# Kernel optimization log

Measured on AMD Instinct MI355X. Metric: run time of the kernel, lower is better.

The kernel has to match this reference:

```python
import jax, jax.numpy as jnp
import numpy as np

# Model dims (ViT-Base @ 384)
L, H, D, HD, M, P, IMG, B, NC, CH = 12, 12, 768, 64, 3072, 16, 384, 32, 1000, 3
NPATCH = (IMG // P) ** 2  # 576
SCALE = 1.0 / np.sqrt(HD)


def setup_inputs() -> dict:
    key = jax.random.key(0)
    ks = iter(jax.random.split(key, 16))
    def n(shape, s=0.02):
        return (jax.random.normal(next(ks), shape, jnp.float32) * s).astype(jnp.float32)
    return dict(
        x=jax.random.normal(next(ks), (B, CH, IMG, IMG), jnp.float32),
        conv_w=n((D, CH, P, P)), conv_b=jnp.zeros((D,), jnp.float32),
        cls_token=jnp.zeros((1, 1, D), jnp.float32),
        pos_emb=n((1, NPATCH + 1, D), 1.0),
        ln1_g=jnp.ones((L, D), jnp.float32), ln1_b=jnp.zeros((L, D), jnp.float32),
        wqkv=n((L, H, D, 3 * HD)), bqkv=jnp.zeros((L, H, 3 * HD), jnp.float32),
        wmsa=n((L, D, D)), bmsa=jnp.zeros((L, D), jnp.float32),
        ln2_g=jnp.ones((L, D), jnp.float32), ln2_b=jnp.zeros((L, D), jnp.float32),
        lnm_g=jnp.ones((L, D), jnp.float32), lnm_b=jnp.zeros((L, D), jnp.float32),
        w1=n((L, D, M)), b1=jnp.zeros((L, M), jnp.float32),
        w2=n((L, M, D)), b2=jnp.zeros((L, D), jnp.float32),
        lnf_g=jnp.ones((D,), jnp.float32), lnf_b=jnp.zeros((D,), jnp.float32),
        whead=n((D, NC)), bhead=jnp.zeros((NC,), jnp.float32),
    )


def _ln(x, g, b, eps=1e-5):
    mu = jnp.mean(x, axis=-1, keepdims=True)
    var = jnp.mean(jnp.square(x - mu), axis=-1, keepdims=True)
    return (x - mu) * jax.lax.rsqrt(var + eps) * g + b


def _encoder_block(x, p):
    (ln1_g, ln1_b, wqkv, bqkv, wmsa, bmsa,
     ln2_g, ln2_b, lnm_g, lnm_b, w1, b1, w2, b2) = p
    b = x.shape[0]
    h = _ln(x, ln1_g, ln1_b)
    # batched per-head QKV (math identical to looping over H small Linears)
    qkv = jnp.einsum('bsd,hde->bhse', h, wqkv) + bqkv[:, None, :]  # [B,H,S,3*HD]
    q, k, v = jnp.split(qkv, 3, axis=-1)
    attn = jax.nn.softmax(jnp.einsum('bhqe,bhke->bhqk', q, k) * SCALE, axis=-1)
    o = jnp.einsum('bhqk,bhke->bhqe', attn, v)          # [B,H,S,HD]
    o = o.transpose(0, 2, 1, 3).reshape(b, -1, D)        # concat heads along feature
    msa = jnp.einsum('bsd,de->bse', o, wmsa) + bmsa
    x1 = h + msa                                          # residual around MSA (post-LN1)
    h2 = _ln(x1, ln2_g, ln2_b)
    h2 = _ln(h2, lnm_g, lnm_b)                            # MLPBlock's own LayerNorm (double LN, faithful)
    mlp = jnp.einsum('bsm,md->bsd', jax.nn.gelu(jnp.einsum('bsd,dm->bsm', h2, w1) + b1, approximate=False), w2) + b2
    return x1 + mlp, None


def reference(x, conv_w, conv_b, cls_token, pos_emb,
              ln1_g, ln1_b, wqkv, bqkv, wmsa, bmsa,
              ln2_g, ln2_b, lnm_g, lnm_b, w1, b1, w2, b2,
              lnf_g, lnf_b, whead, bhead):
    b = x.shape[0]
    # patchify conv (image divisible by patch, so F.pad is a no-op)
    t = jax.lax.conv_general_dilated(x, conv_w, (P, P), 'VALID',
                                     dimension_numbers=('NCHW', 'OIHW', 'NCHW'))
    t = t + conv_b[None, :, None, None]
    # faithful to torch .view(b, -1, embed_dim) on NCHW layout (channel-major flatten)
    t = t.reshape(b, -1, D)
    n = t.shape[1]
    t = jnp.concatenate([jnp.broadcast_to(cls_token, (b, 1, D)), t], axis=1)
    t = t + pos_emb[:, :n + 1]
    stacked = (ln1_g, ln1_b, wqkv, bqkv, wmsa, bmsa,
               ln2_g, ln2_b, lnm_g, lnm_b, w1, b1, w2, b2)
    t, _ = jax.lax.scan(_encoder_block, t, stacked)
    y = _ln(t[:, 0], lnf_g, lnf_b)
    y = jax.nn.softmax(jnp.einsum('bd,dc->bc', y, whead) + bhead, axis=-1)
    return y
```

## Files before the change

kernel.cpp:

```cpp
#include <hip/hip_runtime.h>

using f16   = _Float16;
using f16x8 = __attribute__((ext_vector_type(8))) _Float16;
using f32x4 = __attribute__((ext_vector_type(4))) float;

#define MPAD  18560
#define MREAL 18464
#define MCONV 18432
#define SEQ   577
#define SPAD  640
#define NHEAD 12
#define NBATCH 32
#define SCALE_ 0.125f

__device__ __forceinline__ void load_lds16(const void* g, void* l) {
  __builtin_amdgcn_global_load_lds(
      (const __attribute__((address_space(1))) void*)g,
      (__attribute__((address_space(3))) void*)l, 16, 0, 0);
}

template<int K, int EPI>
__global__ __launch_bounds__(256) void gemm_k(
    const f16* __restrict__ A, const f16* __restrict__ Bt,
    const float* __restrict__ bias, const float* __restrict__ res,
    float* __restrict__ o32, f16* __restrict__ o16a, f16* __restrict__ o16b,
    f16* __restrict__ o16c, const float* __restrict__ pos, int N, int Mreal)
{
  __shared__ __align__(16) f16 As[128*32];
  __shared__ __align__(16) f16 Bs[128*32];
  const int tid = threadIdx.x;
  const int lane = tid & 63, wv = tid >> 6;

  const int gx = gridDim.x, gy = gridDim.y;
  const int nwg = gx * gy;
  const int flat = blockIdx.y * gx + blockIdx.x;
  const int xcd = flat & 7;
  const int qq = nwg >> 3, rr = nwg & 7;
  const int p_ = ((xcd < rr) ? xcd * (qq + 1) : rr * (qq + 1) + (xcd - rr) * qq)
                 + (flat >> 3);
  const int bandsz = gy * 6;
  const int band = p_ / bandsz, within = p_ - band * bandsz;
  const int byi = within / 6;
  const int bxi = band * 6 + (within - byi * 6);
  const int bm = byi << 7, bn = bxi << 7;

  const int wm = (wv >> 1) << 6, wn = (wv & 1) << 6;
  const int r16 = lane & 15, g4 = lane >> 4;
  const f32x4 Z4 = {0.f, 0.f, 0.f, 0.f};

  f32x4 acc[4][4];
#pragma unroll
  for (int m = 0; m < 4; ++m)
#pragma unroll
    for (int n = 0; n < 4; ++n) acc[m][n] = Z4;

  const int soff = wv * 1024 + lane * 8;
  for (int k0 = 0; k0 < K; k0 += 32) {
#pragma unroll
    for (int j = 0; j < 2; ++j) {
      int off = soff + j * 512;
      int row = off >> 5;
      int cs  = (off >> 3) & 3;
      int gc  = cs ^ (row & 3);
      load_lds16(A  + (size_t)(bm + row) * K + k0 + gc * 8, As + (wv*2 + j) * 512);
      load_lds16(Bt + (size_t)(bn + row) * K + k0 + gc * 8, Bs + (wv*2 + j) * 512);
    }
    __syncthreads();
    f16x8 af[4], bf[4];
#pragma unroll
    for (int m = 0; m < 4; ++m) {
      int row = wm + m * 16 + r16;
      af[m] = *(const f16x8*)(As + row * 32 + ((g4 ^ (row & 3)) << 3));
    }
#pragma unroll
    for (int n = 0; n < 4; ++n) {
      int row = wn + n * 16 + r16;
      bf[n] = *(const f16x8*)(Bs + row * 32 + ((g4 ^ (row & 3)) << 3));
    }
#pragma unroll
    for (int m = 0; m < 4; ++m)
#pragma unroll
      for (int n = 0; n < 4; ++n)
        acc[m][n] = __builtin_amdgcn_mfma_f32_16x16x32_f16(af[m], bf[n], acc[m][n], 0, 0, 0);
    __syncthreads();
  }

#pragma unroll
  for (int m = 0; m < 4; ++m) {
#pragma unroll
    for (int n = 0; n < 4; ++n) {
#pragma unroll
      for (int r = 0; r < 4; ++r) {
        int grow = bm + wm + m * 16 + g4 * 4 + r;
        int gcol = bn + wn + n * 16 + r16;
        float v = acc[m][n][r];
        if constexpr (EPI == 0) {
          if (grow < Mreal) {
            int b = grow / 576, p = grow - b * 576;
            int i = gcol * 576 + p;
            int sp = i / 768, dd = i - sp * 768;
            o32[((size_t)(b * SEQ + sp + 1)) * 768 + dd] =
                v + bias[gcol] + pos[(size_t)(sp + 1) * 768 + dd];
          }
        } else if constexpr (EPI == 1) {
          if (grow < Mreal) {
            int b = grow / SEQ, s = grow - b * SEQ;
            int hq = gcol / 192, rem = gcol - hq * 192;
            int sel = rem >> 6, e = rem & 63;
            float val = v + bias[gcol];
            int bh = b * NHEAD + hq;
            if (sel == 0)      o16a[((size_t)bh * SPAD + s) * 64 + e] = (f16)val;
            else if (sel == 1) o16b[((size_t)bh * SPAD + s) * 64 + e] = (f16)val;
            else               o16c[((size_t)bh * 64 + e) * SPAD + s] = (f16)val;
          }
        } else if constexpr (EPI == 2) {
          size_t idx = (size_t)grow * N + gcol;
          o32[idx] = v + bias[gcol] + res[idx];
        } else {
          float val = v + bias[gcol];
          float gl = 0.5f * val * (1.0f + erff(val * 0.70710678f));
          o16a[(size_t)grow * N + gcol] = (f16)gl;
        }
      }
    }
  }
}

__device__ __forceinline__ void block_red2(float& a, float& b, float* sm, int tid) {
  __syncthreads();
#pragma unroll
  for (int d = 32; d; d >>= 1) { a += __shfl_down(a, d); b += __shfl_down(b, d); }
  if ((tid & 63) == 0) { int w = tid >> 6; sm[w] = a; sm[w + 4] = b; }
  __syncthreads();
  a = sm[0] + sm[1] + sm[2] + sm[3];
  b = sm[4] + sm[5] + sm[6] + sm[7];
}

__global__ __launch_bounds__(256) void ln_fwd(const float* __restrict__ X,
    const float* __restrict__ g, const float* __restrict__ bb,
    float* __restrict__ ho, f16* __restrict__ hh)
{
  int row = blockIdx.x, tid = threadIdx.x;
  const float* x = X + (size_t)row * 768;
  float v0 = x[tid], v1 = x[tid + 256], v2 = x[tid + 512];
  float s = v0 + v1 + v2, s2 = v0*v0 + v1*v1 + v2*v2;
  __shared__ float sm[8];
  block_red2(s, s2, sm, tid);
  float mu = s * (1.f/768.f);
  float var = s2 * (1.f/768.f) - mu * mu;
  float rs = rsqrtf(var + 1e-5f);
  size_t base = (size_t)row * 768;
  float y0 = (v0 - mu) * rs * g[tid      ] + bb[tid      ];
  float y1 = (v1 - mu) * rs * g[tid + 256] + bb[tid + 256];
  float y2 = (v2 - mu) * rs * g[tid + 512] + bb[tid + 512];
  ho[base + tid] = y0; ho[base + tid + 256] = y1; ho[base + tid + 512] = y2;
  hh[base + tid] = (f16)y0; hh[base + tid + 256] = (f16)y1; hh[base + tid + 512] = (f16)y2;
}

__global__ __launch_bounds__(256) void ln2_fwd(const float* __restrict__ X,
    const float* __restrict__ g2, const float* __restrict__ bb2,
    const float* __restrict__ gm, const float* __restrict__ bbm,
    f16* __restrict__ hh)
{
  int row = blockIdx.x, tid = threadIdx.x;
  const float* x = X + (size_t)row * 768;
  float v0 = x[tid], v1 = x[tid + 256], v2 = x[tid + 512];
  float s = v0 + v1 + v2, s2 = v0*v0 + v1*v1 + v2*v2;
  __shared__ float sm[8];
  block_red2(s, s2, sm, tid);
  float mu = s * (1.f/768.f), var = s2 * (1.f/768.f) - mu * mu;
  float rs = rsqrtf(var + 1e-5f);
  float y0 = (v0 - mu) * rs * g2[tid      ] + bb2[tid      ];
  float y1 = (v1 - mu) * rs * g2[tid + 256] + bb2[tid + 256];
  float y2 = (v2 - mu) * rs * g2[tid + 512] + bb2[tid + 512];
  s = y0 + y1 + y2; s2 = y0*y0 + y1*y1 + y2*y2;
  block_red2(s, s2, sm, tid);
  mu = s * (1.f/768.f); var = s2 * (1.f/768.f) - mu * mu;
  rs = rsqrtf(var + 1e-5f);
  size_t base = (size_t)row * 768;
  hh[base + tid      ] = (f16)((y0 - mu) * rs * gm[tid      ] + bbm[tid      ]);
  hh[base + tid + 256] = (f16)((y1 - mu) * rs * gm[tid + 256] + bbm[tid + 256]);
  hh[base + tid + 512] = (f16)((y2 - mu) * rs * gm[tid + 512] + bbm[tid + 512]);
}

__global__ __launch_bounds__(256) void attn_k(const f16* __restrict__ qbuf,
    const f16* __restrict__ kbuf, const f16* __restrict__ vtbuf,
    f16* __restrict__ obuf)
{
  const int bh = blockIdx.y;
  const int b = bh / NHEAD, hd = bh - b * NHEAD;
  const int s0 = blockIdx.x << 6;
  const int tid = threadIdx.x, lane = tid & 63, wv = tid >> 6;
  const int r16 = lane & 15, g4 = lane >> 4;
  const f16* Q  = qbuf  + (size_t)bh * SPAD * 64;
  const f16* Kg = kbuf  + (size_t)bh * SPAD * 64;
  const f16* Vg = vtbuf + (size_t)bh * 64 * SPAD;
  __shared__ __align__(16) f16 Kt[64 * 64];
  __shared__ __align__(16) f16 Vt[64 * 64];
  __shared__ __align__(16) f16 Pw[4][16][72];
  const f32x4 Z4 = {0.f, 0.f, 0.f, 0.f};

  f16x8 qf[2];
  {
    const f16* qr = Q + (size_t)(s0 + wv * 16 + r16) * 64;
    qf[0] = *(const f16x8*)(qr + g4 * 8);
    qf[1] = *(const f16x8*)(qr + 32 + g4 * 8);
  }
  float m_run[4] = {-1e30f, -1e30f, -1e30f, -1e30f};
  float l_run[4] = {0.f, 0.f, 0.f, 0.f};
  f32x4 o_acc[4];
#pragma unroll
  for (int n = 0; n < 4; ++n) o_acc[n] = Z4;

  for (int kt = 0; kt < SPAD; kt += 64) {
#pragma unroll
    for (int j = 0; j < 2; ++j) {
      int off = (wv * 2 + j) * 1024 + lane * 16;
      int row = off >> 7;
      int cs  = (off >> 4) & 7;
      int gc  = cs ^ (row & 7);
      load_lds16(Kg + (size_t)(kt + row) * 64 + gc * 8, (void*)((char*)Kt + (wv*2 + j) * 1024));
      load_lds16(Vg + (size_t)row * SPAD + kt + gc * 8, (void*)((char*)Vt + (wv*2 + j) * 1024));
    }
    __syncthreads();

    f32x4 sa[4];
#pragma unroll
    for (int n = 0; n < 4; ++n) sa[n] = Z4;
#pragma unroll
    for (int n = 0; n < 4; ++n) {
      int krow = n * 16 + r16;
#pragma unroll
      for (int kc = 0; kc < 2; ++kc) {
        f16x8 kf = *(const f16x8*)(Kt + krow * 64 + (((kc * 4 + g4) ^ (krow & 7)) << 3));
        sa[n] = __builtin_amdgcn_mfma_f32_16x16x32_f16(qf[kc], kf, sa[n], 0, 0, 0);
      }
    }
#pragma unroll
    for (int r = 0; r < 4; ++r) {
      float mx = -1e30f;
#pragma unroll
      for (int n = 0; n < 4; ++n) {
        int key = kt + n * 16 + r16;
        float sv = (key < SEQ) ? sa[n][r] * SCALE_ : -1e30f;
        sa[n][r] = sv;
        mx = fmaxf(mx, sv);
      }
#pragma unroll
      for (int d = 1; d < 16; d <<= 1) mx = fmaxf(mx, __shfl_xor(mx, d));
      float mnew = fmaxf(m_run[r], mx);
      float alpha = __expf(m_run[r] - mnew);
      m_run[r] = mnew;
      float ssum = 0.f;
#pragma unroll
      for (int n = 0; n < 4; ++n) {
        float p = __expf(sa[n][r] - mnew);
        ssum += p;
        Pw[wv][g4 * 4 + r][n * 16 + r16] = (f16)p;
      }
#pragma unroll
      for (int d = 1; d < 16; d <<= 1) ssum += __shfl_xor(ssum, d);
      l_run[r] = l_run[r] * alpha + ssum;
#pragma unroll
      for (int n = 0; n < 4; ++n) o_acc[n][r] *= alpha;
    }
    f16x8 pf[2];
    pf[0] = *(const f16x8*)(&Pw[wv][r16][g4 * 8]);
    pf[1] = *(const f16x8*)(&Pw[wv][r16][32 + g4 * 8]);
#pragma unroll
    for (int n = 0; n < 4; ++n) {
      int erow = n * 16 + r16;
#pragma unroll
      for (int kc = 0; kc < 2; ++kc) {
        f16x8 vf = *(const f16x8*)(Vt + erow * 64 + (((kc * 4 + g4) ^ (erow & 7)) << 3));
        o_acc[n] = __builtin_amdgcn_mfma_f32_16x16x32_f16(pf[kc], vf, o_acc[n], 0, 0, 0);
      }
    }
    __syncthreads();
  }
  float inv[4];
#pragma unroll
  for (int r = 0; r < 4; ++r) inv[r] = 1.f / l_run[r];
#pragma unroll
  for (int n = 0; n < 4; ++n)
#pragma unroll
    for (int r = 0; r < 4; ++r) {
      int s = s0 + wv * 16 + g4 * 4 + r;
      if (s < SEQ)
        obuf[((size_t)(b * SEQ + s)) * 768 + hd * 64 + n * 16 + r16] =
            (f16)(o_acc[n][r] * inv[r]);
    }
}

__global__ __launch_bounds__(256) void cvt_transpose(const float* __restrict__ in,
    f16* __restrict__ out, int K, int N, size_t ls_in, size_t ls_out)
{
  in  += (size_t)blockIdx.z * ls_in;
  out += (size_t)blockIdx.z * ls_out;
  __shared__ float t[32][33];
  int n0 = blockIdx.x << 5, k0 = blockIdx.y << 5;
  int tx = threadIdx.x & 31, ty = threadIdx.x >> 5;
#pragma unroll
  for (int i = 0; i < 4; ++i) t[ty + 8*i][tx] = in[(size_t)(k0 + ty + 8*i) * N + n0 + tx];
  __syncthreads();
#pragma unroll
  for (int i = 0; i < 4; ++i) out[(size_t)(n0 + ty + 8*i) * K + k0 + tx] = (f16)t[tx][ty + 8*i];
}

__global__ __launch_bounds__(256) void cvt_qkvw(const float* __restrict__ in,
    f16* __restrict__ out, size_t ls_in, size_t ls_out)
{
  in  += (size_t)blockIdx.z * ls_in;
  out += (size_t)blockIdx.z * ls_out;
  __shared__ float t[32][33];
  int n0 = blockIdx.x << 5, k0 = blockIdx.y << 5;
  int tx = threadIdx.x & 31, ty = threadIdx.x >> 5;
  int hq = n0 / 192, r0 = n0 - hq * 192;
#pragma unroll
  for (int i = 0; i < 4; ++i)
    t[ty + 8*i][tx] = in[(size_t)hq * 147456 + (size_t)(k0 + ty + 8*i) * 192 + r0 + tx];
  __syncthreads();
#pragma unroll
  for (int i = 0; i < 4; ++i) out[(size_t)(n0 + ty + 8*i) * 768 + k0 + tx] = (f16)t[tx][ty + 8*i];
}

__global__ __launch_bounds__(256) void cvt_plain(const float* __restrict__ in,
    f16* __restrict__ out, int n)
{
  int i = blockIdx.x * 1024 + threadIdx.x;
#pragma unroll
  for (int j = 0; j < 4; ++j) { int idx = i + j * 256; if (idx < n) out[idx] = (f16)in[idx]; }
}

__global__ __launch_bounds__(256) void zero_vpad(f16* __restrict__ vtb) {
  int bh = blockIdx.x;
  for (int idx = threadIdx.x; idx < 64 * (SPAD - SEQ); idx += 256) {
    int e = idx / (SPAD - SEQ), s = SEQ + idx - e * (SPAD - SEQ);
    vtb[((size_t)bh * 64 + e) * SPAD + s] = (f16)0.f;
  }
}

__global__ __launch_bounds__(256) void im2col_k(const float* __restrict__ x, f16* __restrict__ out) {
  int row = blockIdx.x;
  int b = row / 576, p = row - b * 576;
  int py = p / 24, px = p - py * 24;
  int tid = threadIdx.x;
#pragma unroll
  for (int j = 0; j < 3; ++j) {
    int k = tid + j * 256;
    int c = k >> 8, rem = k & 255;
    int iy = rem >> 4, ix = rem & 15;
    out[(size_t)row * 768 + k] =
        (f16)x[(((size_t)(b * 3 + c)) * 384 + py * 16 + iy) * 384 + px * 16 + ix];
  }
}

__global__ __launch_bounds__(256) void cls_k(const float* __restrict__ ct,
    const float* __restrict__ pos, float* __restrict__ X)
{
  int b = blockIdx.x, tid = threadIdx.x;
#pragma unroll
  for (int j = 0; j < 3; ++j) {
    int d0 = tid + j * 256;
    X[((size_t)b * SEQ) * 768 + d0] = ct[d0] + pos[d0];
  }
}

__global__ __launch_bounds__(256) void head_k(const float* __restrict__ X,
    const float* __restrict__ g, const float* __restrict__ bb,
    const float* __restrict__ W, const float* __restrict__ bhd,
    float* __restrict__ out)
{
  int b = blockIdx.x, tid = threadIdx.x;
  const float* x = X + (size_t)(b * SEQ) * 768;
  float v0 = x[tid], v1 = x[tid + 256], v2 = x[tid + 512];
  float s = v0 + v1 + v2, s2 = v0*v0 + v1*v1 + v2*v2;
  __shared__ float sm[8];
  block_red2(s, s2, sm, tid);
  float mu = s * (1.f/768.f), var = s2 * (1.f/768.f) - mu * mu;
  float rs = rsqrtf(var + 1e-5f);
  __shared__ float y[768];
  y[tid      ] = (v0 - mu) * rs * g[tid      ] + bb[tid      ];
  y[tid + 256] = (v1 - mu) * rs * g[tid + 256] + bb[tid + 256];
  y[tid + 512] = (v2 - mu) * rs * g[tid + 512] + bb[tid + 512];
  __syncthreads();
  float lg[4];
#pragma unroll
  for (int j = 0; j < 4; ++j) {
    int c = tid + j * 256;
    float acc = (c < 1000) ? bhd[c] : -1e30f;
    if (c < 1000)
      for (int d = 0; d < 768; ++d) acc = fmaf(y[d], W[(size_t)d * 1000 + c], acc);
    lg[j] = acc;
  }
  float mx = fmaxf(fmaxf(lg[0], lg[1]), fmaxf(lg[2], lg[3]));
#pragma unroll
  for (int d = 32; d; d >>= 1) mx = fmaxf(mx, __shfl_down(mx, d));
  if ((tid & 63) == 0) sm[tid >> 6] = mx;
  __syncthreads();
  mx = fmaxf(fmaxf(sm[0], sm[1]), fmaxf(sm[2], sm[3]));
  float ex[4], se = 0.f;
#pragma unroll
  for (int j = 0; j < 4; ++j) {
    int c = tid + j * 256;
    ex[j] = (c < 1000) ? __expf(lg[j] - mx) : 0.f;
    se += ex[j];
  }
  __syncthreads();
#pragma unroll
  for (int d = 32; d; d >>= 1) se += __shfl_down(se, d);
  if ((tid & 63) == 0) sm[tid >> 6] = se;
  __syncthreads();
  se = sm[0] + sm[1] + sm[2] + sm[3];
  float inv = 1.f / se;
#pragma unroll
  for (int j = 0; j < 4; ++j) {
    int c = tid + j * 256;
    if (c < 1000) out[(size_t)b * 1000 + c] = ex[j] * inv;
  }
}

extern "C" void kernel_launch(void* const* d_in, const int* in_sizes, int n_in,
                              void* d_out, int out_size, void* d_ws, size_t ws_size,
                              hipStream_t stream)
{
  (void)in_sizes; (void)n_in; (void)out_size;
  const float* x      = (const float*)d_in[0];
  const float* conv_w = (const float*)d_in[1];
  const float* conv_b = (const float*)d_in[2];
  const float* cls_t  = (const float*)d_in[3];
  const float* pos    = (const float*)d_in[4];
  const float* ln1_g  = (const float*)d_in[5];
  const float* ln1_b  = (const float*)d_in[6];
  const float* wqkv   = (const float*)d_in[7];
  const float* bqkv   = (const float*)d_in[8];
  const float* wmsa   = (const float*)d_in[9];
  const float* bmsa   = (const float*)d_in[10];
  const float* ln2_g  = (const float*)d_in[11];
  const float* ln2_b  = (const float*)d_in[12];
  const float* lnm_g  = (const float*)d_in[13];
  const float* lnm_b  = (const float*)d_in[14];
  const float* w1     = (const float*)d_in[15];
  const float* b1     = (const float*)d_in[16];
  const float* w2     = (const float*)d_in[17];
  const float* b2     = (const float*)d_in[18];
  const float* lnf_g  = (const float*)d_in[19];
  const float* lnf_b  = (const float*)d_in[20];
  const float* whead  = (const float*)d_in[21];
  const float* bhead  = (const float*)d_in[22];
  float* out = (float*)d_out;

  const size_t szQ  = (size_t)2304 * 768;
  const size_t szM  = (size_t)768 * 768;
  const size_t szW1 = (size_t)3072 * 768;
  const size_t szW2 = (size_t)768 * 3072;
  const size_t fixed_bytes =
      (size_t)MPAD * 768 * 4 + (size_t)MPAD * 768 * 4 + (size_t)MPAD * 768 * 2 +
      (size_t)MPAD * 3072 * 2 + 3 * ((size_t)NBATCH * NHEAD * SPAD * 64 * 2) +
      (size_t)768 * 768 * 2  + 16 * 256 ;
  const bool hoist =
      ws_size >= fixed_bytes + 12 * (szQ + szM + szW1 + szW2) * 2 + 8 * 256;
  const int LW = hoist ? 12 : 1;

  char* wsp = (char*)d_ws;
  size_t off = 0;
  auto alloc = [&](size_t bytes) {
    char* p = wsp + off; off += (bytes + 255) & ~(size_t)255; return p;
  };
  float* X    = (float*)alloc((size_t)MPAD * 768 * 4);
  float* hbf  = (float*)alloc((size_t)MPAD * 768 * 4);
  f16*   hh   = (f16*)  alloc((size_t)MPAD * 768 * 2);
  f16*   abuf = (f16*)  alloc((size_t)MPAD * 3072 * 2);
  f16*   qb   = (f16*)  alloc((size_t)NBATCH * NHEAD * SPAD * 64 * 2);
  f16*   kb   = (f16*)  alloc((size_t)NBATCH * NHEAD * SPAD * 64 * 2);
  f16*   vtb  = (f16*)  alloc((size_t)NBATCH * NHEAD * SPAD * 64 * 2);
  f16*   WcT  = (f16*)  alloc((size_t)768 * 768 * 2);
  f16*   WqkvT= (f16*)  alloc(LW * szQ  * 2);
  f16*   WmsaT= (f16*)  alloc(LW * szM  * 2);
  f16*   W1T  = (f16*)  alloc(LW * szW1 * 2);
  f16*   W2T  = (f16*)  alloc(LW * szW2 * 2);
  f16*   obuf   = abuf;
  f16*   patchA = abuf;
  f16*   h2h    = hh;
  if (ws_size < off) return;

  zero_vpad<<<dim3(NBATCH * NHEAD), 256, 0, stream>>>(vtb);
  cvt_plain<<<dim3((768 * 768 + 1023) / 1024), 256, 0, stream>>>(conv_w, WcT, 768 * 768);
  if (hoist) {
    cvt_qkvw<<<dim3(72, 24, 12), 256, 0, stream>>>(wqkv, WqkvT, (size_t)12*768*192, szQ);
    cvt_transpose<<<dim3(24, 24, 12), 256, 0, stream>>>(wmsa, WmsaT, 768, 768, szM, szM);
    cvt_transpose<<<dim3(96, 24, 12), 256, 0, stream>>>(w1, W1T, 768, 3072, szW1, szW1);
    cvt_transpose<<<dim3(24, 96, 12), 256, 0, stream>>>(w2, W2T, 3072, 768, szW2, szW2);
  }
  im2col_k<<<dim3(MCONV), 256, 0, stream>>>(x, patchA);
  gemm_k<768, 0><<<dim3(6, 144), 256, 0, stream>>>(
      patchA, WcT, conv_b, nullptr, X, nullptr, nullptr, nullptr, pos, 768, MCONV);
  cls_k<<<dim3(NBATCH), 256, 0, stream>>>(cls_t, pos, X);

  for (int l = 0; l < 12; ++l) {
    f16* wq  = WqkvT + (hoist ? (size_t)l * szQ  : 0);
    f16* wms = WmsaT + (hoist ? (size_t)l * szM  : 0);
    f16* w1t = W1T   + (hoist ? (size_t)l * szW1 : 0);
    f16* w2t = W2T   + (hoist ? (size_t)l * szW2 : 0);
    if (!hoist) {
      cvt_qkvw<<<dim3(72, 24), 256, 0, stream>>>(
          wqkv + (size_t)l * 12 * 768 * 192, wq, 0, 0);
      cvt_transpose<<<dim3(24, 24), 256, 0, stream>>>(
          wmsa + (size_t)l * 768 * 768, wms, 768, 768, 0, 0);
      cvt_transpose<<<dim3(96, 24), 256, 0, stream>>>(
          w1 + (size_t)l * 768 * 3072, w1t, 768, 3072, 0, 0);
      cvt_transpose<<<dim3(24, 96), 256, 0, stream>>>(
          w2 + (size_t)l * 3072 * 768, w2t, 3072, 768, 0, 0);
    }

    ln_fwd<<<dim3(MREAL), 256, 0, stream>>>(X, ln1_g + l * 768, ln1_b + l * 768, hbf, hh);
    gemm_k<768, 1><<<dim3(18, 145), 256, 0, stream>>>(
        hh, wq, bqkv + (size_t)l * 2304, nullptr, nullptr, qb, kb, vtb, nullptr, 2304, MREAL);
    attn_k<<<dim3(10, NBATCH * NHEAD), 256, 0, stream>>>(qb, kb, vtb, obuf);
    gemm_k<768, 2><<<dim3(6, 145), 256, 0, stream>>>(
        obuf, wms, bmsa + l * 768, hbf, X, nullptr, nullptr, nullptr, nullptr, 768, MREAL);
    ln2_fwd<<<dim3(MREAL), 256, 0, stream>>>(
        X, ln2_g + l * 768, ln2_b + l * 768, lnm_g + l * 768, lnm_b + l * 768, h2h);
    gemm_k<768, 3><<<dim3(24, 145), 256, 0, stream>>>(
        h2h, w1t, b1 + (size_t)l * 3072, nullptr, nullptr, abuf, nullptr, nullptr, nullptr, 3072, MREAL);
    gemm_k<3072, 2><<<dim3(6, 145), 256, 0, stream>>>(
        abuf, w2t, b2 + l * 768, X, X, nullptr, nullptr, nullptr, nullptr, 768, MREAL);
  }
  head_k<<<dim3(NBATCH), 256, 0, stream>>>(X, lnf_g, lnf_b, whead, bhead, out);
}
```

Measured before the change: 8.300 ms.

## Recompute LN1 output in MSA epilogue, lazy softmax rescale, split classifier head

LN1 no longer writes its fp32 output. It stores per-row mean and rstd instead, and the MSA projection epilogue rebuilds the normalized residual from X and those stats. This removes a full fp32 activation write and read per layer. Attention now rescales the running max and accumulators only when a new maximum exceeds the old one by more than 8, which skips exp and multiply work on most tiles. The classifier head is split into a logits kernel with more blocks and ILP and a separate softmax kernel, which adds one launch.

```diff
diff --git a/kernel.cpp b/kernel.cpp
--- a/kernel.cpp
+++ b/kernel.cpp
@@ -24,7 +24,9 @@
     const f16* __restrict__ A, const f16* __restrict__ Bt,
     const float* __restrict__ bias, const float* __restrict__ res,
     float* __restrict__ o32, f16* __restrict__ o16a, f16* __restrict__ o16b,
-    f16* __restrict__ o16c, const float* __restrict__ pos, int N, int Mreal)
+    f16* __restrict__ o16c, const float* __restrict__ pos,
+    const float* __restrict__ lng, const float* __restrict__ lnb,
+    const float* __restrict__ stats, int N, int Mreal)
 {
   __shared__ __align__(16) f16 As[128*32];
   __shared__ __align__(16) f16 Bs[128*32];
@@ -116,6 +118,13 @@
         } else if constexpr (EPI == 2) {
           size_t idx = (size_t)grow * N + gcol;
           o32[idx] = v + bias[gcol] + res[idx];
+        } else if constexpr (EPI == 4) {
+          if (grow < Mreal) {
+            size_t idx = (size_t)grow * N + gcol;
+            float mu = stats[2 * grow], rs = stats[2 * grow + 1];
+            float h = (res[idx] - mu) * rs * lng[gcol] + lnb[gcol];
+            o32[idx] = v + bias[gcol] + h;
+          }
         } else {
           float val = v + bias[gcol];
           float gl = 0.5f * val * (1.0f + erff(val * 0.70710678f));
@@ -138,7 +147,7 @@
 
 __global__ __launch_bounds__(256) void ln_fwd(const float* __restrict__ X,
     const float* __restrict__ g, const float* __restrict__ bb,
-    float* __restrict__ ho, f16* __restrict__ hh)
+    float* __restrict__ stats, f16* __restrict__ hh)
 {
   int row = blockIdx.x, tid = threadIdx.x;
   const float* x = X + (size_t)row * 768;
@@ -149,12 +158,11 @@
   float mu = s * (1.f/768.f);
   float var = s2 * (1.f/768.f) - mu * mu;
   float rs = rsqrtf(var + 1e-5f);
+  if (tid == 0) { stats[2 * row] = mu; stats[2 * row + 1] = rs; }
   size_t base = (size_t)row * 768;
-  float y0 = (v0 - mu) * rs * g[tid      ] + bb[tid      ];
-  float y1 = (v1 - mu) * rs * g[tid + 256] + bb[tid + 256];
-  float y2 = (v2 - mu) * rs * g[tid + 512] + bb[tid + 512];
-  ho[base + tid] = y0; ho[base + tid + 256] = y1; ho[base + tid + 512] = y2;
-  hh[base + tid] = (f16)y0; hh[base + tid + 256] = (f16)y1; hh[base + tid + 512] = (f16)y2;
+  hh[base + tid      ] = (f16)((v0 - mu) * rs * g[tid      ] + bb[tid      ]);
+  hh[base + tid + 256] = (f16)((v1 - mu) * rs * g[tid + 256] + bb[tid + 256]);
+  hh[base + tid + 512] = (f16)((v2 - mu) * rs * g[tid + 512] + bb[tid + 512]);
 }
 
 __global__ __launch_bounds__(256) void ln2_fwd(const float* __restrict__ X,
@@ -248,21 +256,24 @@
       }
 #pragma unroll
       for (int d = 1; d < 16; d <<= 1) mx = fmaxf(mx, __shfl_xor(mx, d));
-      float mnew = fmaxf(m_run[r], mx);
-      float alpha = __expf(m_run[r] - mnew);
-      m_run[r] = mnew;
+      if (!__all(mx - m_run[r] <= 8.f)) {
+        float mnew = fmaxf(m_run[r], mx);
+        float alpha = __expf(m_run[r] - mnew);
+        m_run[r] = mnew;
+        l_run[r] *= alpha;
+#pragma unroll
+        for (int n = 0; n < 4; ++n) o_acc[n][r] *= alpha;
+      }
       float ssum = 0.f;
 #pragma unroll
       for (int n = 0; n < 4; ++n) {
-        float p = __expf(sa[n][r] - mnew);
+        float p = __expf(sa[n][r] - m_run[r]);
         ssum += p;
         Pw[wv][g4 * 4 + r][n * 16 + r16] = (f16)p;
       }
 #pragma unroll
       for (int d = 1; d < 16; d <<= 1) ssum += __shfl_xor(ssum, d);
-      l_run[r] = l_run[r] * alpha + ssum;
-#pragma unroll
-      for (int n = 0; n < 4; ++n) o_acc[n][r] *= alpha;
+      l_run[r] += ssum;
     }
     f16x8 pf[2];
     pf[0] = *(const f16x8*)(&Pw[wv][r16][g4 * 8]);
@@ -366,10 +377,10 @@
   }
 }
 
-__global__ __launch_bounds__(256) void head_k(const float* __restrict__ X,
+__global__ __launch_bounds__(256) void head_logits(const float* __restrict__ X,
     const float* __restrict__ g, const float* __restrict__ bb,
     const float* __restrict__ W, const float* __restrict__ bhd,
-    float* __restrict__ out)
+    float* __restrict__ lg)
 {
   int b = blockIdx.x, tid = threadIdx.x;
   const float* x = X + (size_t)(b * SEQ) * 768;
@@ -384,26 +395,42 @@
   y[tid + 256] = (v1 - mu) * rs * g[tid + 256] + bb[tid + 256];
   y[tid + 512] = (v2 - mu) * rs * g[tid + 512] + bb[tid + 512];
   __syncthreads();
-  float lg[4];
+  int c = blockIdx.y * 250 + tid;
+  if (tid < 250) {
+    float a0 = 0.f, a1 = 0.f, a2 = 0.f, a3 = 0.f;
+#pragma unroll 4
+    for (int d = 0; d < 768; d += 4) {
+      a0 = fmaf(y[d    ], W[(size_t)(d    ) * 1000 + c], a0);
+      a1 = fmaf(y[d + 1], W[(size_t)(d + 1) * 1000 + c], a1);
+      a2 = fmaf(y[d + 2], W[(size_t)(d + 2) * 1000 + c], a2);
+      a3 = fmaf(y[d + 3], W[(size_t)(d + 3) * 1000 + c], a3);
+    }
+    lg[(size_t)b * 1000 + c] = (a0 + a1) + (a2 + a3) + bhd[c];
+  }
+}
+
+__global__ __launch_bounds__(256) void head_soft(const float* __restrict__ lg,
+    float* __restrict__ out)
+{
+  int b = blockIdx.x, tid = threadIdx.x;
+  __shared__ float sm[8];
+  float v[4], mx = -1e30f;
 #pragma unroll
   for (int j = 0; j < 4; ++j) {
     int c = tid + j * 256;
-    float acc = (c < 1000) ? bhd[c] : -1e30f;
-    if (c < 1000)
-      for (int d = 0; d < 768; ++d) acc = fmaf(y[d], W[(size_t)d * 1000 + c], acc);
-    lg[j] = acc;
-  }
-  float mx = fmaxf(fmaxf(lg[0], lg[1]), fmaxf(lg[2], lg[3]));
+    v[j] = (c < 1000) ? lg[(size_t)b * 1000 + c] : -1e30f;
+    mx = fmaxf(mx, v[j]);
+  }
 #pragma unroll
   for (int d = 32; d; d >>= 1) mx = fmaxf(mx, __shfl_down(mx, d));
   if ((tid & 63) == 0) sm[tid >> 6] = mx;
   __syncthreads();
   mx = fmaxf(fmaxf(sm[0], sm[1]), fmaxf(sm[2], sm[3]));
-  float ex[4], se = 0.f;
+  float se = 0.f, ex[4];
 #pragma unroll
   for (int j = 0; j < 4; ++j) {
     int c = tid + j * 256;
-    ex[j] = (c < 1000) ? __expf(lg[j] - mx) : 0.f;
+    ex[j] = (c < 1000) ? __expf(v[j] - mx) : 0.f;
     se += ex[j];
   }
   __syncthreads();
@@ -455,7 +482,8 @@
   const size_t szW1 = (size_t)3072 * 768;
   const size_t szW2 = (size_t)768 * 3072;
   const size_t fixed_bytes =
-      (size_t)MPAD * 768 * 4 + (size_t)MPAD * 768 * 4 + (size_t)MPAD * 768 * 2 +
+      (size_t)MPAD * 768 * 4 + (size_t)MPAD * 8 + 32 * 1000 * 4 +
+      (size_t)MPAD * 768 * 2 +
       (size_t)MPAD * 3072 * 2 + 3 * ((size_t)NBATCH * NHEAD * SPAD * 64 * 2) +
       (size_t)768 * 768 * 2  + 16 * 256 ;
   const bool hoist =
@@ -468,7 +496,8 @@
     char* p = wsp + off; off += (bytes + 255) & ~(size_t)255; return p;
   };
   float* X    = (float*)alloc((size_t)MPAD * 768 * 4);
-  float* hbf  = (float*)alloc((size_t)MPAD * 768 * 4);
+  float* stats= (float*)alloc((size_t)MPAD * 8);
+  float* lgbuf= (float*)alloc((size_t)32 * 1000 * 4);
   f16*   hh   = (f16*)  alloc((size_t)MPAD * 768 * 2);
   f16*   abuf = (f16*)  alloc((size_t)MPAD * 3072 * 2);
   f16*   qb   = (f16*)  alloc((size_t)NBATCH * NHEAD * SPAD * 64 * 2);
@@ -494,7 +523,8 @@
   }
   im2col_k<<<dim3(MCONV), 256, 0, stream>>>(x, patchA);
   gemm_k<768, 0><<<dim3(6, 144), 256, 0, stream>>>(
-      patchA, WcT, conv_b, nullptr, X, nullptr, nullptr, nullptr, pos, 768, MCONV);
+      patchA, WcT, conv_b, nullptr, X, nullptr, nullptr, nullptr, pos,
+      nullptr, nullptr, nullptr, 768, MCONV);
   cls_k<<<dim3(NBATCH), 256, 0, stream>>>(cls_t, pos, X);
 
   for (int l = 0; l < 12; ++l) {
@@ -513,18 +543,23 @@
           w2 + (size_t)l * 3072 * 768, w2t, 3072, 768, 0, 0);
     }
 
-    ln_fwd<<<dim3(MREAL), 256, 0, stream>>>(X, ln1_g + l * 768, ln1_b + l * 768, hbf, hh);
+    ln_fwd<<<dim3(MREAL), 256, 0, stream>>>(X, ln1_g + l * 768, ln1_b + l * 768, stats, hh);
     gemm_k<768, 1><<<dim3(18, 145), 256, 0, stream>>>(
-        hh, wq, bqkv + (size_t)l * 2304, nullptr, nullptr, qb, kb, vtb, nullptr, 2304, MREAL);
+        hh, wq, bqkv + (size_t)l * 2304, nullptr, nullptr, qb, kb, vtb, nullptr,
+        nullptr, nullptr, nullptr, 2304, MREAL);
     attn_k<<<dim3(10, NBATCH * NHEAD), 256, 0, stream>>>(qb, kb, vtb, obuf);
-    gemm_k<768, 2><<<dim3(6, 145), 256, 0, stream>>>(
-        obuf, wms, bmsa + l * 768, hbf, X, nullptr, nullptr, nullptr, nullptr, 768, MREAL);
+    gemm_k<768, 4><<<dim3(6, 145), 256, 0, stream>>>(
+        obuf, wms, bmsa + l * 768, X, X, nullptr, nullptr, nullptr, nullptr,
+        ln1_g + l * 768, ln1_b + l * 768, stats, 768, MREAL);
     ln2_fwd<<<dim3(MREAL), 256, 0, stream>>>(
         X, ln2_g + l * 768, ln2_b + l * 768, lnm_g + l * 768, lnm_b + l * 768, h2h);
     gemm_k<768, 3><<<dim3(24, 145), 256, 0, stream>>>(
-        h2h, w1t, b1 + (size_t)l * 3072, nullptr, nullptr, abuf, nullptr, nullptr, nullptr, 3072, MREAL);
+        h2h, w1t, b1 + (size_t)l * 3072, nullptr, nullptr, abuf, nullptr, nullptr, nullptr,
+        nullptr, nullptr, nullptr, 3072, MREAL);
     gemm_k<3072, 2><<<dim3(6, 145), 256, 0, stream>>>(
-        abuf, w2t, b2 + l * 768, X, X, nullptr, nullptr, nullptr, nullptr, 768, MREAL);
-  }
-  head_k<<<dim3(NBATCH), 256, 0, stream>>>(X, lnf_g, lnf_b, whead, bhead, out);
-}
+        abuf, w2t, b2 + l * 768, X, X, nullptr, nullptr, nullptr, nullptr,
+        nullptr, nullptr, nullptr, 768, MREAL);
+  }
+  head_logits<<<dim3(NBATCH, 4), 256, 0, stream>>>(X, lnf_g, lnf_b, whead, bhead, lgbuf);
+  head_soft<<<dim3(NBATCH), 256, 0, stream>>>(lgbuf, out);
+}
```

Measured after the change: 8.434 ms. No clear change (+1.6%).
